# Performance work log

Measured on AMD Instinct MI355X. Metric: run time of the kernel, lower is better.

## Reference

```python
import jax, jax.numpy as jnp
import numpy as np

EPS = 1e-5  # BatchNorm eps (torch default)


def _norm_adj(adj):
    # DenseGCNConv: add self-loops, symmetric degree normalization
    N = adj.shape[-1]
    adj = adj + jnp.eye(N, dtype=adj.dtype)
    d = jnp.clip(adj.sum(-1), 1.0, None) ** -0.5
    return d[..., :, None] * adj * d[..., None, :]


def _gcn(x, adj_norm, W, b):
    return jnp.einsum('bij,bjf->bif', adj_norm, x @ W) + b


def _batchnorm(h, gamma, beta):
    # torch BatchNorm1d in training mode over flattened (B*N, C)
    B, N, C = h.shape
    hf = h.reshape(B * N, C)
    mu = hf.mean(0)
    var = hf.var(0)  # biased, as used for normalization
    out = (hf - mu) * jax.lax.rsqrt(var + EPS) * gamma + beta
    return out.reshape(B, N, C)


def setup_inputs() -> dict:
    key = jax.random.key(0)
    ks = jax.random.split(key, 24)
    B, N, F, H, D = 4, 256, 6, 128, 256
    s = 0.05
    a = jax.random.uniform(ks[1], (B, N, N), dtype=jnp.float32)
    adj = ((a + jnp.swapaxes(a, 1, 2)) / 2 < 0.1).astype(jnp.float32)  # sparse symmetric adjacency
    return {
        'x': jax.random.normal(ks[0], (B, N, F), dtype=jnp.float32),
        'adj': adj,
        'W1': jax.random.normal(ks[2], (F, H)) * s, 'b1': jnp.zeros((H,)),
        'W2': jax.random.normal(ks[3], (H, H)) * s, 'b2': jnp.zeros((H,)),
        'W3': jax.random.normal(ks[4], (H, D)) * s, 'b3': jnp.zeros((D,)),
        'g1': jnp.ones((H,)), 'beta1': jnp.zeros((H,)),
        'g2': jnp.ones((H,)), 'beta2': jnp.zeros((H,)),
        'e1w': jax.random.normal(ks[5], (2 * D, H)) * s, 'e1b': jnp.zeros((H,)),
        'e2w': jax.random.normal(ks[6], (H, H // 2)) * s, 'e2b': jnp.zeros((H // 2,)),
        'e3w': jax.random.normal(ks[7], (H // 2, 1)) * s, 'e3b': jnp.zeros((1,)),
        'f1w': jax.random.normal(ks[8], (D, H)) * s, 'f1b': jnp.zeros((H,)),
        'f2w': jax.random.normal(ks[9], (H, H)) * s, 'f2b': jnp.zeros((H,)),
        'f3w': jax.random.normal(ks[10], (H, F)) * s, 'f3b': jnp.zeros((F,)),
    }


def reference(x, adj, W1, b1, W2, b2, W3, b3, g1, beta1, g2, beta2,
              e1w, e1b, e2w, e2b, e3w, e3b, f1w, f1b, f2w, f2b, f3w, f3b):
    adj_norm = _norm_adj(adj)
    h = jax.nn.relu(_batchnorm(_gcn(x, adj_norm, W1, b1), g1, beta1))
    h = jax.nn.relu(_batchnorm(_gcn(h, adj_norm, W2, b2), g2, beta2))
    h = jax.nn.relu(_gcn(h, adj_norm, W3, b3))  # [B,N,D]
    D = h.shape[-1]
    # AdjacencyDecoder: Linear(cat(h_i,h_j)) == h_i@e1w[:D] + h_j@e1w[D:] (fused form, same math)
    hi = h @ e1w[:D]   # [B,N,H]
    hj = h @ e1w[D:]   # [B,N,H]
    p = jax.nn.relu(hi[:, :, None, :] + hj[:, None, :, :] + e1b)  # [B,N,N,H]
    p = jax.nn.relu(p @ e2w + e2b)                                 # [B,N,N,H/2]
    logits = (p @ e3w + e3b)[..., 0]                               # [B,N,N]
    logits = (logits + jnp.swapaxes(logits, 1, 2)) / 2
    adj_pred = jax.nn.sigmoid(logits)
    # FeatureDecoder
    f = jax.nn.relu(h @ f1w + f1b)
    f = jax.nn.relu(f @ f2w + f2b)
    feat_pred = f @ f3w + f3b
    return adj_pred, feat_pred
```

## Files before the change

kernel.cpp:

```cpp
#include <hip/hip_runtime.h>


typedef float v4f __attribute__((ext_vector_type(4)));
typedef short v8s __attribute__((ext_vector_type(8)));

__device__ __forceinline__ unsigned short f2bs(float f) {
    union { float f; unsigned int u; } v;
    v.f = f;
    return (unsigned short)((v.u + 0x7fffu + ((v.u >> 16) & 1u)) >> 16);
}

__global__ void k_pre(const float* x, const float* W1, const float* adj,
                      const float* e2w, float* buf, float* dg,
                      unsigned short* bfr_g) {
    __shared__ float ss[256];
    int blk = blockIdx.x, tid = threadIdx.x;
    if (blk < 512) {
        int idx = blk * 256 + tid;
        int m = idx >> 7, n = idx & 127;
        float s = 0.f;
        for (int k = 0; k < 6; k++) s += x[m * 6 + k] * W1[k * 128 + n];
        buf[idx] = s;
    } else if (blk < 768) {
        int row = (blk - 512) * 4 + (tid >> 6);
        int lane = tid & 63;
        const float* ap = adj + (long)row * 256;
        ss[tid] = ap[lane] + ap[lane + 64] + ap[lane + 128] + ap[lane + 192];
        __syncthreads();
        for (int o = 32; o > 0; o >>= 1) {
            if (lane < o) ss[tid] += ss[tid + o];
            __syncthreads();
        }
        if (lane == 0) {
            float t = ss[tid] + 1.f;
            if (t < 1.f) t = 1.f;
            dg[row] = rsqrtf(t);
        }
    } else {
        for (int s = tid; s < 8192; s += 256) {
            int k = s >> 6, n = s & 63;
            int kc = k >> 5, q = (k & 31) >> 3, t = k & 7;
            int nt = n >> 4, c2 = n & 15;
            bfr_g[(((nt * 4 + kc) * 64) + q * 16 + c2) * 8 + t] = f2bs(e2w[s]);
        }
    }
}

__global__ void k_an(const float* adj, const float* dg, float* An) {
    for (int p = 0; p < 2; p++) {
        int idx = blockIdx.x * 256 + threadIdx.x + p * 131072;
        int b = idx >> 16, i = (idx >> 8) & 255, j = idx & 255;
        float v = adj[idx] + ((i == j) ? 1.f : 0.f);
        An[idx] = dg[b * 256 + i] * v * dg[b * 256 + j];
    }
}

__device__ void dev_tile(int t, const float* A, const float* B, const float* bias,
                         const float* stat, const float* g, const float* beta,
                         float* ostat, float* C,
                         int K, int N, int relu,
                         int sA, int sB, int sC, int tiles_n, int tiles_m,
                         float* smem) {
    float* As = smem;
    float* Bs = smem + 272;
    int tid = threadIdx.x;
    int n2 = tid & 15, ml = tid >> 4;
    int bx = t % tiles_n;
    int tmp = t / tiles_n;
    int by = tmp % tiles_m;
    int bz = tmp / tiles_m;
    int m0 = by * 16, n0 = bx * 32;
    const float* Ab = A + (long)bz * sA;
    const float* Bb = B + (long)bz * sB;
    float* Cb = C + (long)bz * sC;
    float c0 = 0.f, c1 = 0.f;
    for (int k0 = 0; k0 < K; k0 += 16) {
        int kk = tid & 15, mm = tid >> 4;
        int kg = k0 + kk;
        float v = Ab[(long)(m0 + mm) * K + kg];
        if (stat != 0) {
            float mu = stat[kg] * (1.f / 1024.f);
            float vr = stat[128 + kg] * (1.f / 1024.f) - mu * mu;
            float sc = rsqrtf(vr + 1e-5f) * g[kg];
            v = (v - mu) * sc + beta[kg];
            if (v < 0.f) v = 0.f;
        }
        As[kk * 17 + mm] = v;
        int nn2 = tid & 31, kk2 = tid >> 5;
        Bs[kk2 * 33 + nn2] = Bb[(long)(k0 + kk2) * N + n0 + nn2];
        int idx = tid + 256;
        nn2 = idx & 31; kk2 = idx >> 5;
        Bs[kk2 * 33 + nn2] = Bb[(long)(k0 + kk2) * N + n0 + nn2];
        __syncthreads();
        #pragma unroll
        for (int q = 0; q < 16; q++) {
            float a = As[q * 17 + ml];
            float b0 = Bs[q * 33 + n2 * 2];
            float b1 = Bs[q * 33 + n2 * 2 + 1];
            c0 += a * b0; c1 += a * b1;
        }
        __syncthreads();
    }
    int mRow = m0 + ml, nn = n0 + n2 * 2;
    if (bias != 0) { c0 += bias[nn]; c1 += bias[nn + 1]; }
    if (relu) {
        if (c0 < 0.f) c0 = 0.f;
        if (c1 < 0.f) c1 = 0.f;
    }
    Cb[(long)mRow * N + nn] = c0;
    Cb[(long)mRow * N + nn + 1] = c1;

    if (ostat != 0) {
        float* sred = smem + 800;
        float* qred = smem + 1344;
        __syncthreads();
        sred[(n2 * 2) * 17 + ml] = c0;
        sred[(n2 * 2 + 1) * 17 + ml] = c1;
        qred[(n2 * 2) * 17 + ml] = c0 * c0;
        qred[(n2 * 2 + 1) * 17 + ml] = c1 * c1;
        __syncthreads();
        if (tid < 32) {
            float s = 0.f, q = 0.f;
            for (int u = 0; u < 16; u++) {
                s += sred[tid * 17 + u];
                q += qred[tid * 17 + u];
            }
            atomicAdd(&ostat[n0 + tid], s);
            atomicAdd(&ostat[128 + n0 + tid], q);
        }
    }
}

__global__ void k_tgemm(const float* A, const float* B, const float* bias,
                        const float* stat, const float* g, const float* beta,
                        float* ostat, float* C,
                        int K, int N, int relu,
                        int sA, int sB, int sC, int tiles_n, int tiles_m) {
    __shared__ float smem[1888];
    dev_tile(blockIdx.x, A, B, bias, stat, g, beta, ostat, C,
             K, N, relu, sA, sB, sC, tiles_n, tiles_m, smem);
}

__global__ void k_g67(const float* hb, const float* e1w, float* hi,
                      const float* f1w, const float* f1b, float* f1) {
    __shared__ float smem[1888];
    int t = blockIdx.x;
    if (t < 512) {
        dev_tile(t, hb, e1w, 0, 0, 0, 0, 0, hi,
                 256, 128, 0, 0, 32768, 131072, 4, 64, smem);
    } else {
        dev_tile(t - 512, hb, f1w, f1b, 0, 0, 0, 0, f1,
                 256, 128, 1, 0, 0, 0, 4, 64, smem);
    }
}

__global__ void k_decf(const float* hi, const float* hj, const float* e1b,
                       const unsigned short* bfr_g, const float* e2b,
                       const float* e3w, const float* e3b,
                       const float* f1, const float* f2w, const float* f2b_,
                       const float* f3w, const float* f3b,
                       float* lg, float* out) {
    __shared__ float smem[4608];
    int tid = threadIdx.x;
    int blk = blockIdx.x;
    if (blk < 1024) {
        float* red = smem;
        float* pre_sh = smem + 4352;
        int lane = tid & 63, wv = tid >> 6;
        int col = lane & 15, quad = lane >> 4;
        int bi = blk, b = bi >> 8;
        if (tid < 128) pre_sh[tid] = hi[bi * 128 + tid] + e1b[tid];
        __syncthreads();
        float preR[4][8];
        for (int kc = 0; kc < 4; kc++)
            for (int t = 0; t < 8; t++)
                preR[kc][t] = pre_sh[kc * 32 + quad * 8 + t];
        v4f acc[4][4];
        for (int ms = 0; ms < 4; ms++)
            for (int nt = 0; nt < 4; nt++) {
                v4f z = {0.f, 0.f, 0.f, 0.f};
                acc[ms][nt] = z;
            }
        const float* hjb = hj + b * 32768;
        for (int kc = 0; kc < 4; kc++) {
            v8s bfrag[4];
            for (int nt = 0; nt < 4; nt++)
                bfrag[nt] = *(const v8s*)&bfr_g[(((nt * 4 + kc) * 64) + lane) * 8];
            for (int ms = 0; ms < 4; ms++) {
                int j = wv * 64 + ms * 16 + col;
                const float* hp = hjb + j * 128 + kc * 32 + quad * 8;
                v8s af;
                for (int t = 0; t < 8; t++) {
                    float p = preR[kc][t] + hp[t];
                    p = (p > 0.f) ? p : 0.f;
                    af[t] = (short)f2bs(p);
                }
                for (int nt = 0; nt < 4; nt++)
                    acc[ms][nt] = __builtin_amdgcn_mfma_f32_16x16x32_bf16(
                        af, bfrag[nt], acc[ms][nt], 0, 0, 0);
            }
        }
        float e2bv[4], e3wv[4];
        for (int nt = 0; nt < 4; nt++) {
            e2bv[nt] = e2b[nt * 16 + col];
            e3wv[nt] = e3w[nt * 16 + col];
        }
        for (int ms = 0; ms < 4; ms++) {
            for (int r = 0; r < 4; r++) {
                float s = 0.f;
                for (int nt = 0; nt < 4; nt++) {
                    float v = acc[ms][nt][r] + e2bv[nt];
                    if (v > 0.f) s += v * e3wv[nt];
                }
                red[(wv * 64 + ms * 16 + quad * 4 + r) * 17 + col] = s;
            }
        }
        __syncthreads();
        float s = e3b[0];
        for (int c = 0; c < 16; c++) s += red[tid * 17 + c];
        lg[bi * 256 + tid] = s;
    } else {
        float* f2row = smem;
        int r0 = (blk - 1024) * 4;
        for (int p = 0; p < 2; p++) {
            int idx = tid + p * 256;
            int r = r0 + (idx >> 7), n = idx & 127;
            float s = f2b_[n];
            const float* f1r = f1 + (long)r * 128;
            for (int k = 0; k < 128; k++) s += f1r[k] * f2w[k * 128 + n];
            if (s < 0.f) s = 0.f;
            f2row[idx] = s;
        }
        __syncthreads();
        if (tid < 24) {
            int r = tid / 6, c = tid % 6;
            float s = f3b[c];
            const float* fr = f2row + r * 128;
            for (int k = 0; k < 128; k++) s += fr[k] * f3w[k * 6 + c];
            out[262144 + (r0 + r) * 6 + c] = s;
        }
    }
}

__global__ void k_symsig(const float* lg, float* out) {
    for (int p = 0; p < 2; p++) {
        int idx = blockIdx.x * 256 + threadIdx.x + p * 131072;
        int b = idx >> 16, i = (idx >> 8) & 255, j = idx & 255;
        float v = 0.5f * (lg[idx] + lg[(b << 16) + (j << 8) + i]);
        out[idx] = 1.f / (1.f + expf(-v));
    }
}

extern "C" void kernel_launch(void* const* d_in, const int* in_sizes, int n_in,
                              void* d_out, int out_size, void* d_ws, size_t ws_size,
                              hipStream_t stream) {
    const float* x   = (const float*)d_in[0];
    const float* adj = (const float*)d_in[1];
    const float* W1  = (const float*)d_in[2];
    const float* b1  = (const float*)d_in[3];
    const float* W2  = (const float*)d_in[4];
    const float* b2  = (const float*)d_in[5];
    const float* W3  = (const float*)d_in[6];
    const float* b3  = (const float*)d_in[7];
    const float* g1  = (const float*)d_in[8];
    const float* be1 = (const float*)d_in[9];
    const float* g2  = (const float*)d_in[10];
    const float* be2 = (const float*)d_in[11];
    const float* e1w = (const float*)d_in[12];
    const float* e1b = (const float*)d_in[13];
    const float* e2w = (const float*)d_in[14];
    const float* e2b = (const float*)d_in[15];
    const float* e3w = (const float*)d_in[16];
    const float* e3b = (const float*)d_in[17];
    const float* f1w = (const float*)d_in[18];
    const float* f1b = (const float*)d_in[19];
    const float* f2w = (const float*)d_in[20];
    const float* f2b_ = (const float*)d_in[21];
    const float* f3w = (const float*)d_in[22];
    const float* f3b = (const float*)d_in[23];

    float* out = (float*)d_out;

    if (ws_size < (size_t)1600000 * 4) {
        hipMemsetAsync(d_out, 0x60, 4096, stream);
        return;
    }
    float* ws = (float*)d_ws;
    float* st1 = ws;
    float* st2 = ws + 256;
    float* dg  = ws + 512;
    unsigned short* bfr_g = (unsigned short*)(ws + 1536);
    float* An  = ws + 5632;
    float* buf = An + 262144;
    float* hb  = buf + 262144;
    float* lg  = hb + 262144;
    float* h1  = lg + 262144;
    float* h2  = h1 + 131072;
    float* hi  = h2 + 131072;
    float* hj  = hi + 131072;

    hipMemsetAsync(st1, 0, 512 * sizeof(float), stream);

    k_pre<<<769, 256, 0, stream>>>(x, W1, adj, e2w, buf, dg, bfr_g);
    k_an<<<512, 256, 0, stream>>>(adj, dg, An);
    k_tgemm<<<256, 256, 0, stream>>>(An, buf, b1, 0, 0, 0, st1, h1,
                                     256, 128, 0, 65536, 32768, 32768, 4, 16);
    k_tgemm<<<256, 256, 0, stream>>>(h1, W2, 0, st1, g1, be1, 0, buf,
                                     128, 128, 0, 0, 0, 0, 4, 64);
    k_tgemm<<<256, 256, 0, stream>>>(An, buf, b2, 0, 0, 0, st2, h2,
                                     256, 128, 0, 65536, 32768, 32768, 4, 16);
    k_tgemm<<<512, 256, 0, stream>>>(h2, W3, 0, st2, g2, be2, 0, buf,
                                     128, 256, 0, 0, 0, 0, 8, 64);
    k_tgemm<<<512, 256, 0, stream>>>(An, buf, b3, 0, 0, 0, 0, hb,
                                     256, 256, 1, 65536, 65536, 65536, 8, 16);
    k_g67<<<768, 256, 0, stream>>>(hb, e1w, hi, f1w, f1b, h1);
    k_decf<<<1280, 256, 0, stream>>>(hi, hj, e1b, bfr_g, e2b, e3w, e3b,
                                     h1, f2w, f2b_, f3w, f3b, lg, out);
    k_symsig<<<512, 256, 0, stream>>>(lg, out);
}
```

Measured before the change: 219.9 us.

## Fold adjacency normalization into GCN aggregation GEMMs and drop separate An kernel

Removes the kernel that materializes the normalized adjacency matrix. The aggregation GEMMs now read the raw adjacency, add the self-loop on the diagonal while loading the A tile, scale B rows by the column degree factor, and scale output rows by the row degree factor. The stats memset is also folded into the preprocessing kernel's last block. This saves two launches and one full N×N write and read pass, at the cost of a few extra multiplies and branches in the GEMM inner load.

```diff
diff --git a/kernel.cpp b/kernel.cpp
--- a/kernel.cpp
+++ b/kernel.cpp
@@ -12,7 +12,7 @@
 
 __global__ void k_pre(const float* x, const float* W1, const float* adj,
                       const float* e2w, float* buf, float* dg,
-                      unsigned short* bfr_g) {
+                      unsigned short* bfr_g, float* st) {
     __shared__ float ss[256];
     int blk = blockIdx.x, tid = threadIdx.x;
     if (blk < 512) {
@@ -43,19 +43,13 @@
             int nt = n >> 4, c2 = n & 15;
             bfr_g[(((nt * 4 + kc) * 64) + q * 16 + c2) * 8 + t] = f2bs(e2w[s]);
         }
-    }
-}
-
-__global__ void k_an(const float* adj, const float* dg, float* An) {
-    for (int p = 0; p < 2; p++) {
-        int idx = blockIdx.x * 256 + threadIdx.x + p * 131072;
-        int b = idx >> 16, i = (idx >> 8) & 255, j = idx & 255;
-        float v = adj[idx] + ((i == j) ? 1.f : 0.f);
-        An[idx] = dg[b * 256 + i] * v * dg[b * 256 + j];
+        st[tid] = 0.f;
+        st[256 + tid] = 0.f;
     }
 }
 
 __device__ void dev_tile(int t, const float* A, const float* B, const float* bias,
+                         const float* dgA,
                          const float* stat, const float* g, const float* beta,
                          float* ostat, float* C,
                          int K, int N, int relu,
@@ -73,12 +67,15 @@
     const float* Ab = A + (long)bz * sA;
     const float* Bb = B + (long)bz * sB;
     float* Cb = C + (long)bz * sC;
+    const float* dgb = (dgA != 0) ? (dgA + bz * 256) : 0;
     float c0 = 0.f, c1 = 0.f;
     for (int k0 = 0; k0 < K; k0 += 16) {
         int kk = tid & 15, mm = tid >> 4;
         int kg = k0 + kk;
         float v = Ab[(long)(m0 + mm) * K + kg];
-        if (stat != 0) {
+        if (dgA != 0) {
+            if (m0 + mm == kg) v += 1.f;
+        } else if (stat != 0) {
             float mu = stat[kg] * (1.f / 1024.f);
             float vr = stat[128 + kg] * (1.f / 1024.f) - mu * mu;
             float sc = rsqrtf(vr + 1e-5f) * g[kg];
@@ -87,10 +84,14 @@
         }
         As[kk * 17 + mm] = v;
         int nn2 = tid & 31, kk2 = tid >> 5;
-        Bs[kk2 * 33 + nn2] = Bb[(long)(k0 + kk2) * N + n0 + nn2];
+        float w = Bb[(long)(k0 + kk2) * N + n0 + nn2];
+        if (dgA != 0) w *= dgb[k0 + kk2];
+        Bs[kk2 * 33 + nn2] = w;
         int idx = tid + 256;
         nn2 = idx & 31; kk2 = idx >> 5;
-        Bs[kk2 * 33 + nn2] = Bb[(long)(k0 + kk2) * N + n0 + nn2];
+        w = Bb[(long)(k0 + kk2) * N + n0 + nn2];
+        if (dgA != 0) w *= dgb[k0 + kk2];
+        Bs[kk2 * 33 + nn2] = w;
         __syncthreads();
         #pragma unroll
         for (int q = 0; q < 16; q++) {
@@ -102,6 +103,10 @@
         __syncthreads();
     }
     int mRow = m0 + ml, nn = n0 + n2 * 2;
+    if (dgA != 0) {
+        float dm = dgb[mRow];
+        c0 *= dm; c1 *= dm;
+    }
     if (bias != 0) { c0 += bias[nn]; c1 += bias[nn + 1]; }
     if (relu) {
         if (c0 < 0.f) c0 = 0.f;
@@ -132,12 +137,13 @@
 }
 
 __global__ void k_tgemm(const float* A, const float* B, const float* bias,
+                        const float* dgA,
                         const float* stat, const float* g, const float* beta,
                         float* ostat, float* C,
                         int K, int N, int relu,
                         int sA, int sB, int sC, int tiles_n, int tiles_m) {
     __shared__ float smem[1888];
-    dev_tile(blockIdx.x, A, B, bias, stat, g, beta, ostat, C,
+    dev_tile(blockIdx.x, A, B, bias, dgA, stat, g, beta, ostat, C,
              K, N, relu, sA, sB, sC, tiles_n, tiles_m, smem);
 }
 
@@ -146,10 +152,10 @@
     __shared__ float smem[1888];
     int t = blockIdx.x;
     if (t < 512) {
-        dev_tile(t, hb, e1w, 0, 0, 0, 0, 0, hi,
+        dev_tile(t, hb, e1w, 0, 0, 0, 0, 0, 0, hi,
                  256, 128, 0, 0, 32768, 131072, 4, 64, smem);
     } else {
-        dev_tile(t - 512, hb, f1w, f1b, 0, 0, 0, 0, f1,
+        dev_tile(t - 512, hb, f1w, f1b, 0, 0, 0, 0, 0, f1,
                  256, 128, 1, 0, 0, 0, 4, 64, smem);
     }
 }
@@ -281,7 +287,7 @@
 
     float* out = (float*)d_out;
 
-    if (ws_size < (size_t)1600000 * 4) {
+    if (ws_size < (size_t)1400000 * 4) {
         hipMemsetAsync(d_out, 0x60, 4096, stream);
         return;
     }
@@ -290,8 +296,7 @@
     float* st2 = ws + 256;
     float* dg  = ws + 512;
     unsigned short* bfr_g = (unsigned short*)(ws + 1536);
-    float* An  = ws + 5632;
-    float* buf = An + 262144;
+    float* buf = ws + 5632;
     float* hb  = buf + 262144;
     float* lg  = hb + 262144;
     float* h1  = lg + 262144;
@@ -299,19 +304,16 @@
     float* hi  = h2 + 131072;
     float* hj  = hi + 131072;
 
-    hipMemsetAsync(st1, 0, 512 * sizeof(float), stream);
-
-    k_pre<<<769, 256, 0, stream>>>(x, W1, adj, e2w, buf, dg, bfr_g);
-    k_an<<<512, 256, 0, stream>>>(adj, dg, An);
-    k_tgemm<<<256, 256, 0, stream>>>(An, buf, b1, 0, 0, 0, st1, h1,
+    k_pre<<<769, 256, 0, stream>>>(x, W1, adj, e2w, buf, dg, bfr_g, st1);
+    k_tgemm<<<256, 256, 0, stream>>>(adj, buf, b1, dg, 0, 0, 0, st1, h1,
                                      256, 128, 0, 65536, 32768, 32768, 4, 16);
-    k_tgemm<<<256, 256, 0, stream>>>(h1, W2, 0, st1, g1, be1, 0, buf,
+    k_tgemm<<<256, 256, 0, stream>>>(h1, W2, 0, 0, st1, g1, be1, 0, buf,
                                      128, 128, 0, 0, 0, 0, 4, 64);
-    k_tgemm<<<256, 256, 0, stream>>>(An, buf, b2, 0, 0, 0, st2, h2,
+    k_tgemm<<<256, 256, 0, stream>>>(adj, buf, b2, dg, 0, 0, 0, st2, h2,
                                      256, 128, 0, 65536, 32768, 32768, 4, 16);
-    k_tgemm<<<512, 256, 0, stream>>>(h2, W3, 0, st2, g2, be2, 0, buf,
+    k_tgemm<<<512, 256, 0, stream>>>(h2, W3, 0, 0, st2, g2, be2, 0, buf,
                                      128, 256, 0, 0, 0, 0, 8, 64);
-    k_tgemm<<<512, 256, 0, stream>>>(An, buf, b3, 0, 0, 0, 0, hb,
+    k_tgemm<<<512, 256, 0, stream>>>(adj, buf, b3, dg, 0, 0, 0, 0, hb,
                                      256, 256, 1, 65536, 65536, 65536, 8, 16);
     k_g67<<<768, 256, 0, stream>>>(hb, e1w, hi, f1w, f1b, h1);
     k_decf<<<1280, 256, 0, stream>>>(hi, hj, e1b, bfr_g, e2b, e3w, e3b,
```

Result: slower. 232.2 us (+5.6%).
